# Kernel tuning notes

Hardware: AMD Instinct MI355X
Metric: run time of the kernel (lower is better)

Reference implementation:

```python
import jax, jax.numpy as jnp
import numpy as np

R_S, R_T = 16, 8
D_SEG, D_GLB = 64, 128
H_SEG, H_GLB = 2, 4
NL = 2
FF_SEG, FF_GLB = 128, 256
THRESH = 0.5
B, L = 16, 1024


def setup_inputs() -> dict:
    key = jax.random.key(0)
    ks = iter(jax.random.split(key, 40))

    def p(shape, s=0.02):
        return s * jax.random.normal(next(ks), shape, dtype=jnp.float32)

    inp = {}
    inp['pts'] = jax.random.normal(next(ks), (B, L, 3), dtype=jnp.float32)
    # Fourier spatio-temporal encoder params
    inp['fs'] = p((2, R_S), 1.0)                      # spatial frequencies
    inp['ft'] = p((R_T,), 1.0)                        # temporal frequencies
    inp['w_space'] = p((2 * R_S, D_SEG)); inp['b_space'] = p((D_SEG,))
    inp['w_time'] = p((2 * R_T, 32)); inp['b_time'] = p((32,))
    inp['w_fout'] = p((D_SEG + 32, D_SEG)); inp['b_fout'] = p((D_SEG,))
    # gating
    inp['w_gate'] = p((D_SEG,), 1.0); inp['b_gate'] = p(())
    # segment mini-transformer (2 post-norm encoder layers, relu FFN)
    inp['seg_attn_w'] = p((NL, 4, D_SEG, D_SEG)); inp['seg_attn_b'] = p((NL, 4, D_SEG))
    inp['seg_ln_g'] = jnp.ones((NL, 2, D_SEG), jnp.float32)
    inp['seg_ln_b'] = jnp.zeros((NL, 2, D_SEG), jnp.float32)
    inp['seg_ff1_w'] = p((NL, D_SEG, FF_SEG)); inp['seg_ff1_b'] = p((NL, FF_SEG))
    inp['seg_ff2_w'] = p((NL, FF_SEG, D_SEG)); inp['seg_ff2_b'] = p((NL, D_SEG))
    # global aggregator transformer
    inp['glb_attn_w'] = p((NL, 4, D_GLB, D_GLB)); inp['glb_attn_b'] = p((NL, 4, D_GLB))
    inp['glb_ln_g'] = jnp.ones((NL, 2, D_GLB), jnp.float32)
    inp['glb_ln_b'] = jnp.zeros((NL, 2, D_GLB), jnp.float32)
    inp['glb_ff1_w'] = p((NL, D_GLB, FF_GLB)); inp['glb_ff1_b'] = p((NL, FF_GLB))
    inp['glb_ff2_w'] = p((NL, FF_GLB, D_GLB)); inp['glb_ff2_b'] = p((NL, D_GLB))
    # projections
    inp['up_w'] = p((D_SEG, D_GLB)); inp['up_b'] = p((D_GLB,))
    inp['fin_w'] = p((D_GLB, D_GLB)); inp['fin_b'] = p((D_GLB,))
    return inp


def _ln(x, g, b, eps=1e-5):
    m = x.mean(-1, keepdims=True)
    v = ((x - m) ** 2).mean(-1, keepdims=True)
    return (x - m) * jax.lax.rsqrt(v + eps) * g + b


def _mha(x, mask, w, bb, nh):
    Bb, S, D = x.shape
    hd = D // nh
    wq, wk, wv, wo = w
    bq, bk, bv, bo = bb
    q = (x @ wq + bq).reshape(Bb, S, nh, hd)
    k = (x @ wk + bk).reshape(Bb, S, nh, hd)
    v = (x @ wv + bv).reshape(Bb, S, nh, hd)
    sc = jnp.einsum('bqhd,bkhd->bhqk', q, k) / jnp.sqrt(jnp.float32(hd))
    sc = jnp.where(mask[:, None, :, :], sc, jnp.float32(-1e9))
    a = jax.nn.softmax(sc, axis=-1)
    o = jnp.einsum('bhqk,bkhd->bqhd', a, v).reshape(Bb, S, D)
    return o @ wo + bo


def _encoder(x, mask, attn_w, attn_b, ln_g, ln_b, ff1_w, ff1_b, ff2_w, ff2_b, nh):
    # PyTorch-style post-norm TransformerEncoder (dropout=0, eval mode)
    for l in range(attn_w.shape[0]):
        x = _ln(x + _mha(x, mask, attn_w[l], attn_b[l], nh), ln_g[l, 0], ln_b[l, 0])
        h = jax.nn.relu(x @ ff1_w[l] + ff1_b[l]) @ ff2_w[l] + ff2_b[l]
        x = _ln(x + h, ln_g[l, 1], ln_b[l, 1])
    return x


def reference(pts, fs, ft, w_space, b_space, w_time, b_time, w_fout, b_fout, w_gate, b_gate, seg_attn_w, seg_attn_b, seg_ln_g, seg_ln_b, seg_ff1_w, seg_ff1_b, seg_ff2_w, seg_ff2_b, glb_attn_w, glb_attn_b, glb_ln_g, glb_ln_b, glb_ff1_w, glb_ff1_b, glb_ff2_w, glb_ff2_b, up_w, up_b, fin_w, fin_b):
    Bb, Ll, _ = pts.shape
    two_pi = jnp.float32(2.0 * np.pi)
    xy, t = pts[..., :2], pts[..., 2:3]
    # Fourier features (space + time), fused into d=64 point embedding z
    sp = xy @ fs * two_pi                                        # [B,L,r_s]
    sp_feat = jnp.concatenate([jnp.sin(sp), jnp.cos(sp)], -1) @ w_space + b_space
    tp = t * ft * two_pi                                         # [B,L,r_t]
    t_feat = jnp.concatenate([jnp.sin(tp), jnp.cos(tp)], -1) @ w_time + b_time
    z = jnp.concatenate([sp_feat, t_feat], -1) @ w_fout + b_fout  # [B,L,64]

    # dynamic segmentation gating: boundary where sigmoid gate > threshold
    gate = jax.nn.sigmoid(z @ w_gate + b_gate)                   # [B,L]
    boundary = (gate > THRESH).at[:, 0].set(True)
    seg_id = jnp.cumsum(boundary.astype(jnp.int32), axis=1) - 1  # [B,L] contiguous ids
    n_seg = seg_id[:, -1] + 1                                    # [B]

    # segment mini-transformer == full-length transformer with within-segment attention mask
    seg_mask = seg_id[:, :, None] == seg_id[:, None, :]          # [B,L,L]
    h = _encoder(z, seg_mask, seg_attn_w, seg_attn_b, seg_ln_g, seg_ln_b,
                 seg_ff1_w, seg_ff1_b, seg_ff2_w, seg_ff2_b, H_SEG)

    # per-segment mean pooling (padded to L segment slots)
    sums = jax.vmap(lambda hh, sid: jax.ops.segment_sum(hh, sid, num_segments=Ll))(h, seg_id)
    cnts = jax.vmap(lambda sid: jax.ops.segment_sum(jnp.ones((Ll,), jnp.float32), sid, num_segments=Ll))(seg_id)
    seg_emb = sums / jnp.maximum(cnts, 1.0)[..., None]           # [B,L,64]
    valid = jnp.arange(Ll)[None, :] < n_seg[:, None]             # [B,L]
    seg_emb = jnp.where(valid[..., None], seg_emb @ up_w + up_b, 0.0)  # [B,L,128]

    # global aggregator over valid segment embeddings (padding-masked)
    glb_mask = (valid[:, None, :] & valid[:, :, None]) | jnp.eye(Ll, dtype=bool)[None]
    g = _encoder(seg_emb, glb_mask, glb_attn_w, glb_attn_b, glb_ln_g, glb_ln_b,
                 glb_ff1_w, glb_ff1_b, glb_ff2_w, glb_ff2_b, H_GLB)
    agg = (g * valid[..., None]).sum(1) / n_seg[:, None].astype(jnp.float32)

    # single-segment trajectories skip the global aggregator
    global_emb = jnp.where((n_seg == 1)[:, None], seg_emb[:, 0, :], agg)
    return global_emb @ fin_w + fin_b                            # [B,128]
```

## Files before the change

kernel.cpp:

```cpp
#include <hip/hip_runtime.h>
#include <math.h>

#define B_ 16
#define L_ 1024
#define M_TOT (B_*L_)

typedef __attribute__((ext_vector_type(8))) short short8v;
typedef __attribute__((ext_vector_type(4))) float f32x4;

__device__ __forceinline__ float wave_reduce_sum(float v) {
#pragma unroll
  for (int o = 32; o >= 1; o >>= 1) v += __shfl_xor(v, o, 64);
  return v;
}

__device__ __forceinline__ unsigned short f2bf(float f) {
  union { float f; unsigned u; } v; v.f = f;
  unsigned r = v.u + 0x7FFFu + ((v.u >> 16) & 1u);
  return (unsigned short)(r >> 16);
}

__global__ __launch_bounds__(256) void pack_all_kernel(
    const float* __restrict__ s0, const float* __restrict__ s1,
    const float* __restrict__ s2, const float* __restrict__ s3,
    const float* __restrict__ s4, const float* __restrict__ s5,
    const float* __restrict__ s6, unsigned short* __restrict__ wpk)
{
  int idx = blockIdx.x*256 + (int)threadIdx.x;
  const float* src; unsigned short* dst; int K, N;
  if      (idx <  4096) { src=s0; dst=wpk;          K=64;  N=64;  }
  else if (idx <  6144) { src=s1; dst=wpk+32768;    K=64;  N=128; idx-=4096; }
  else if (idx <  8192) { src=s2; dst=wpk+49152;    K=128; N=64;  idx-=6144; }
  else if (idx < 24576) { src=s3; dst=wpk+65536;    K=128; N=128; idx-=8192; }
  else if (idx < 32768) { src=s4; dst=wpk+196608;   K=128; N=256; idx-=24576; }
  else if (idx < 40960) { src=s5; dst=wpk+262144;   K=256; N=128; idx-=32768; }
  else if (idx < 41984) { src=s6; dst=wpk+327680;   K=64;  N=128; idx-=40960; }
  else return;
  const int l = idx & 63;
  int f = idx >> 6;
  const int ntn = N >> 4;
  const int nt = f % ntn; f /= ntn;
  const int ktn = K >> 5;
  const int kt = f % ktn;
  const int m  = f / ktn;
  const float* s = src + (size_t)m*K*N + (size_t)(kt*32 + ((l>>4)<<3))*N + nt*16 + (l&15);
  unsigned pw[4];
#pragma unroll
  for (int jj = 0; jj < 4; ++jj)
    pw[jj] = (unsigned)f2bf(s[(size_t)(2*jj)*N]) | ((unsigned)f2bf(s[(size_t)(2*jj+1)*N]) << 16);
  uint4 u; u.x = pw[0]; u.y = pw[1]; u.z = pw[2]; u.w = pw[3];
  *reinterpret_cast<uint4*>(dst + (size_t)idx*8) = u;
}

template<int K, int PN, int NPARTS, bool RELU, bool GATED, bool WF32, bool WBF,
         int SPART = -1, bool SEMB0 = false>
__global__ __launch_bounds__(256) void mgemm_kernel(
    const unsigned short* __restrict__ Abf,
    const unsigned short* __restrict__ Wpk,
    const float* __restrict__ bias,
    float* __restrict__ C, unsigned short* __restrict__ Cbf,
    const int* __restrict__ nseg, float* __restrict__ semb0)
{
  constexpr int NOUT = NPARTS*PN;
  constexpr int KT = K/32;
  constexpr int NTP = PN/16;
  constexpr int CPP = PN/64;
  const int row0 = blockIdx.x * 64;
  if (GATED) { const int b = row0 >> 10; if ((row0 & (L_-1)) >= nseg[b]) return; }
  const int ct = blockIdx.y;
  const int part = ct / CPP;
  const int nt0  = (ct % CPP) * 4;
  const int wv = (int)threadIdx.x >> 6;
  const int ln = (int)threadIdx.x & 63;
  const int rbase = row0 + wv*16;
  const unsigned short* aptr = Abf + (size_t)(rbase + (ln & 15))*K + ((ln >> 4) << 3);
  const unsigned short* bptr = Wpk + ((size_t)part*KT*NTP + nt0)*512 + (size_t)ln*8;
  f32x4 acc0 = {0.f,0.f,0.f,0.f}, acc1 = {0.f,0.f,0.f,0.f};
  f32x4 acc2 = {0.f,0.f,0.f,0.f}, acc3 = {0.f,0.f,0.f,0.f};
#pragma unroll
  for (int kt = 0; kt < KT; ++kt) {
    short8v a = *reinterpret_cast<const short8v*>(aptr + kt*32);
    const unsigned short* bk = bptr + (size_t)kt*NTP*512;
    short8v b0 = *reinterpret_cast<const short8v*>(bk);
    short8v b1 = *reinterpret_cast<const short8v*>(bk + 512);
    short8v b2 = *reinterpret_cast<const short8v*>(bk + 1024);
    short8v b3 = *reinterpret_cast<const short8v*>(bk + 1536);
    acc0 = __builtin_amdgcn_mfma_f32_16x16x32_bf16(a, b0, acc0, 0, 0, 0);
    acc1 = __builtin_amdgcn_mfma_f32_16x16x32_bf16(a, b1, acc1, 0, 0, 0);
    acc2 = __builtin_amdgcn_mfma_f32_16x16x32_bf16(a, b2, acc2, 0, 0, 0);
    acc3 = __builtin_amdgcn_mfma_f32_16x16x32_bf16(a, b3, acc3, 0, 0, 0);
  }
  const int colb = part*PN + nt0*16 + (ln & 15);
  const int rowe = rbase + ((ln >> 4) << 2);
  f32x4 av[4] = {acc0, acc1, acc2, acc3};
#pragma unroll
  for (int i = 0; i < 4; ++i) {
    const int col = colb + i*16;
    const float bs = bias[col];
#pragma unroll
    for (int r = 0; r < 4; ++r) {
      float v = av[i][r] + bs;
      if (SPART >= 0) { if (part == SPART) v *= 0.25506972533f; }
      if (RELU) v = fmaxf(v, 0.f);
      const int row = rowe + r;
      if (WF32) C[(size_t)row*NOUT + col] = v;
      if (WBF)  Cbf[(size_t)row*NOUT + col] = f2bf(v);
      if (SEMB0) { if ((row & (L_-1)) == 0) semb0[(row >> 10)*NOUT + col] = v; }
    }
  }
}

__global__ __launch_bounds__(256) void mgemm_qkvfrag_kernel(
    const unsigned short* __restrict__ Abf,
    const unsigned short* __restrict__ Wpk,
    const float* __restrict__ bias,
    unsigned short* __restrict__ qbf,
    unsigned short* __restrict__ kfrag,
    unsigned short* __restrict__ vfrag,
    const int* __restrict__ nseg)
{
  constexpr int K = 128, PN = 128, KT = 4, NTP = 8;
  const int row0 = blockIdx.x * 64;
  const int bb = row0 >> 10;
  if ((row0 & (L_-1)) >= nseg[bb]) return;
  const int ct = blockIdx.y;
  const int part = ct >> 1;
  const int nt0 = (ct & 1) * 4;
  const int wv = (int)threadIdx.x >> 6;
  const int ln = (int)threadIdx.x & 63;
  const int qc = ln & 15;
  const int rbase = row0 + wv*16;
  const unsigned short* aptr = Abf + (size_t)(rbase + qc)*K + ((ln >> 4) << 3);
  const unsigned short* bptr = Wpk + ((size_t)part*KT*NTP + nt0)*512 + (size_t)ln*8;
  f32x4 acc[4];
#pragma unroll
  for (int i = 0; i < 4; ++i) acc[i] = f32x4{0.f,0.f,0.f,0.f};
#pragma unroll
  for (int kt = 0; kt < KT; ++kt) {
    short8v a = *reinterpret_cast<const short8v*>(aptr + kt*32);
    const unsigned short* bk = bptr + (size_t)kt*NTP*512;
#pragma unroll
    for (int i = 0; i < 4; ++i)
      acc[i] = __builtin_amdgcn_mfma_f32_16x16x32_bf16(
          a, *reinterpret_cast<const short8v*>(bk + i*512), acc[i], 0, 0, 0);
  }
  const int rowe = rbase + ((ln >> 4) << 2);
#pragma unroll
  for (int i = 0; i < 4; ++i) {
    const int cl = (nt0 + i)*16 + qc;
    const int h = cl >> 5, dh = cl & 31;
    const float bs = bias[part*PN + cl];
#pragma unroll
    for (int r = 0; r < 4; ++r) {
      float v = acc[i][r] + bs;
      const int row = rowe + r;
      const int key = row & (L_-1);
      if (part == 0) {
        v *= 0.25506972533f;
        qbf[(size_t)row*128 + cl] = f2bf(v);
      } else if (part == 1) {
        const size_t idx = (((size_t)((bb*4 + h)*32 + (key>>5))*2 + ((key>>4)&1))*64
                            + ((dh>>3)*16 + (key&15)))*8 + (dh&7);
        kfrag[idx] = f2bf(v);
      } else {
        const int kk = key & 31;
        const size_t idx = (((size_t)((bb*4 + h)*32 + (key>>5))*2 + (dh>>4))*64
                            + (((kk&15)>>2)*16 + (dh&15)))*8 + ((kk>>4)*4 + (kk&3));
        vfrag[idx] = f2bf(v);
      }
    }
  }
}

template<int K>
__global__ __launch_bounds__(256) void mgemm_ln64_kernel(
    const unsigned short* __restrict__ Abf,
    const unsigned short* __restrict__ Wpk,
    const float* __restrict__ bias,
    float* __restrict__ x,
    const float* __restrict__ gam, const float* __restrict__ bet,
    unsigned short* __restrict__ xbf)
{
  constexpr int KT = K/32;
  const int row0 = blockIdx.x * 64;
  const int wv = (int)threadIdx.x >> 6;
  const int ln = (int)threadIdx.x & 63;
  const int rbase = row0 + wv*16;
  const unsigned short* aptr = Abf + (size_t)(rbase + (ln & 15))*K + ((ln >> 4) << 3);
  const unsigned short* bptr = Wpk + (size_t)ln*8;
  f32x4 acc0 = {0.f,0.f,0.f,0.f}, acc1 = {0.f,0.f,0.f,0.f};
  f32x4 acc2 = {0.f,0.f,0.f,0.f}, acc3 = {0.f,0.f,0.f,0.f};
#pragma unroll
  for (int kt = 0; kt < KT; ++kt) {
    short8v a = *reinterpret_cast<const short8v*>(aptr + kt*32);
    const unsigned short* bk = bptr + (size_t)kt*4*512;
    short8v b0 = *reinterpret_cast<const short8v*>(bk);
    short8v b1 = *reinterpret_cast<const short8v*>(bk + 512);
    short8v b2 = *reinterpret_cast<const short8v*>(bk + 1024);
    short8v b3 = *reinterpret_cast<const short8v*>(bk + 1536);
    acc0 = __builtin_amdgcn_mfma_f32_16x16x32_bf16(a, b0, acc0, 0, 0, 0);
    acc1 = __builtin_amdgcn_mfma_f32_16x16x32_bf16(a, b1, acc1, 0, 0, 0);
    acc2 = __builtin_amdgcn_mfma_f32_16x16x32_bf16(a, b2, acc2, 0, 0, 0);
    acc3 = __builtin_amdgcn_mfma_f32_16x16x32_bf16(a, b3, acc3, 0, 0, 0);
  }
  const int colc = ln & 15;
  const int rowe = rbase + ((ln >> 4) << 2);
  f32x4 av[4] = {acc0, acc1, acc2, acc3};
  float v[4][4];
#pragma unroll
  for (int i = 0; i < 4; ++i) {
    const int col = i*16 + colc;
    const float bs = bias[col];
#pragma unroll
    for (int r = 0; r < 4; ++r)
      v[i][r] = av[i][r] + bs + x[(size_t)(rowe + r)*64 + col];
  }
  float rs[4];
#pragma unroll
  for (int r = 0; r < 4; ++r) rs[r] = v[0][r]+v[1][r]+v[2][r]+v[3][r];
#pragma unroll
  for (int m = 1; m <= 8; m <<= 1)
#pragma unroll
    for (int r = 0; r < 4; ++r) rs[r] += __shfl_xor(rs[r], m, 64);
  float mean[4], vs[4];
#pragma unroll
  for (int r = 0; r < 4; ++r) { mean[r] = rs[r]*(1.0f/64.0f); vs[r] = 0.f; }
#pragma unroll
  for (int i = 0; i < 4; ++i)
#pragma unroll
    for (int r = 0; r < 4; ++r) { const float d = v[i][r]-mean[r]; vs[r] = fmaf(d, d, vs[r]); }
#pragma unroll
  for (int m = 1; m <= 8; m <<= 1)
#pragma unroll
    for (int r = 0; r < 4; ++r) vs[r] += __shfl_xor(vs[r], m, 64);
  float rstd[4];
#pragma unroll
  for (int r = 0; r < 4; ++r) rstd[r] = rsqrtf(vs[r]*(1.0f/64.0f) + 1e-5f);
#pragma unroll
  for (int i = 0; i < 4; ++i) {
    const int col = i*16 + colc;
    const float g = gam[col], bb = bet[col];
#pragma unroll
    for (int r = 0; r < 4; ++r) {
      const float out = (v[i][r]-mean[r])*rstd[r]*g + bb;
      x[(size_t)(rowe + r)*64 + col] = out;
      xbf[(size_t)(rowe + r)*64 + col] = f2bf(out);
    }
  }
}

template<int K>
__global__ __launch_bounds__(256) void mgemm_ln128_kernel(
    const unsigned short* __restrict__ Abf,
    const unsigned short* __restrict__ Wpk,
    const float* __restrict__ bias,
    float* __restrict__ x,
    const float* __restrict__ gam, const float* __restrict__ bet,
    const int* __restrict__ nseg, unsigned short* __restrict__ xbf)
{
  constexpr int KT = K/32;
  const int row0 = blockIdx.x * 64;
  if ((row0 & (L_-1)) >= nseg[row0 >> 10]) return;
  const int wv = (int)threadIdx.x >> 6;
  const int ln = (int)threadIdx.x & 63;
  const int qc = ln & 15;
  const int rbase = row0 + wv*16;
  const unsigned short* aptr = Abf + (size_t)(rbase + qc)*K + ((ln >> 4) << 3);
  const unsigned short* bptr = Wpk + (size_t)ln*8;
  f32x4 acc[8];
#pragma unroll
  for (int i = 0; i < 8; ++i) acc[i] = f32x4{0.f,0.f,0.f,0.f};
#pragma unroll
  for (int kt = 0; kt < KT; ++kt) {
    short8v a = *reinterpret_cast<const short8v*>(aptr + kt*32);
    const unsigned short* bk = bptr + (size_t)kt*8*512;
#pragma unroll
    for (int i = 0; i < 8; ++i)
      acc[i] = __builtin_amdgcn_mfma_f32_16x16x32_bf16(
          a, *reinterpret_cast<const short8v*>(bk + i*512), acc[i], 0, 0, 0);
  }
  const int rowe = rbase + ((ln >> 4) << 2);
  float v[8][4];
#pragma unroll
  for (int i = 0; i < 8; ++i) {
    const int col = i*16 + qc;
    const float bs = bias[col];
#pragma unroll
    for (int r = 0; r < 4; ++r)
      v[i][r] = acc[i][r] + bs + x[(size_t)(rowe + r)*128 + col];
  }
  float rs[4];
#pragma unroll
  for (int r = 0; r < 4; ++r)
    rs[r] = ((v[0][r]+v[1][r])+(v[2][r]+v[3][r])) + ((v[4][r]+v[5][r])+(v[6][r]+v[7][r]));
#pragma unroll
  for (int m = 1; m <= 8; m <<= 1)
#pragma unroll
    for (int r = 0; r < 4; ++r) rs[r] += __shfl_xor(rs[r], m, 64);
  float mean[4], vs[4];
#pragma unroll
  for (int r = 0; r < 4; ++r) { mean[r] = rs[r]*(1.0f/128.0f); vs[r] = 0.f; }
#pragma unroll
  for (int i = 0; i < 8; ++i)
#pragma unroll
    for (int r = 0; r < 4; ++r) { const float d = v[i][r]-mean[r]; vs[r] = fmaf(d, d, vs[r]); }
#pragma unroll
  for (int m = 1; m <= 8; m <<= 1)
#pragma unroll
    for (int r = 0; r < 4; ++r) vs[r] += __shfl_xor(vs[r], m, 64);
  float rstd[4];
#pragma unroll
  for (int r = 0; r < 4; ++r) rstd[r] = rsqrtf(vs[r]*(1.0f/128.0f) + 1e-5f);
#pragma unroll
  for (int i = 0; i < 8; ++i) {
    const int col = i*16 + qc;
    const float g = gam[col], bb = bet[col];
#pragma unroll
    for (int r = 0; r < 4; ++r) {
      const float out = (v[i][r]-mean[r])*rstd[r]*g + bb;
      x[(size_t)(rowe + r)*128 + col] = out;
      xbf[(size_t)(rowe + r)*128 + col] = f2bf(out);
    }
  }
}

__global__ __launch_bounds__(256) void featurize_kernel(
    const float* __restrict__ pts, const float* __restrict__ fs, const float* __restrict__ ft,
    const float* __restrict__ w_space, const float* __restrict__ b_space,
    const float* __restrict__ w_time, const float* __restrict__ b_time,
    const float* __restrict__ w_fout, const float* __restrict__ b_fout,
    const float* __restrict__ w_gate, const float* __restrict__ b_gate,
    float* __restrict__ z, unsigned short* __restrict__ zbf, int* __restrict__ boundary)
{
  const int sub = threadIdx.x >> 6;
  const int d   = threadIdx.x & 63;
  const int p   = blockIdx.x * 4 + sub;
  const float TWO_PI = 6.283185307179586f;
  __shared__ float feat[4][32];
  __shared__ float tfeat[4][16];
  __shared__ float g96[4][96];
  const float x = pts[p*3+0], y = pts[p*3+1], t = pts[p*3+2];
  if (d < 16) {
    float sp = (x*fs[d] + y*fs[16+d]) * TWO_PI;
    feat[sub][d]    = sinf(sp);
    feat[sub][16+d] = cosf(sp);
  } else if (d < 24) {
    int r = d - 16;
    float tp = t * ft[r] * TWO_PI;
    tfeat[sub][r]   = sinf(tp);
    tfeat[sub][8+r] = cosf(tp);
  }
  __syncthreads();
  float sf = b_space[d];
#pragma unroll
  for (int k2 = 0; k2 < 32; ++k2) sf = fmaf(feat[sub][k2], w_space[k2*64+d], sf);
  g96[sub][d] = sf;
  if (d < 32) {
    float tf = b_time[d];
#pragma unroll
    for (int k2 = 0; k2 < 16; ++k2) tf = fmaf(tfeat[sub][k2], w_time[k2*32+d], tf);
    g96[sub][64+d] = tf;
  }
  __syncthreads();
  float zv = b_fout[d];
#pragma unroll
  for (int k2 = 0; k2 < 96; ++k2) zv = fmaf(g96[sub][k2], w_fout[k2*64+d], zv);
  z[(size_t)p*64+d] = zv;
  zbf[(size_t)p*64+d] = f2bf(zv);
  float gv = wave_reduce_sum(zv * w_gate[d]);
  if (d == 0) {
    float logit = gv + b_gate[0];
    float gate = 1.0f / (1.0f + expf(-logit));
    int bnd = (gate > 0.5f) ? 1 : 0;
    if ((p & (L_-1)) == 0) bnd = 1;
    boundary[p] = bnd;
  }
}

__global__ __launch_bounds__(1024) void scan_kernel(const int* __restrict__ boundary,
    int* __restrict__ seg_id, int* __restrict__ seg_start, int* __restrict__ n_seg)
{
  __shared__ int sc[1024];
  const int b = blockIdx.x, l = threadIdx.x;
  const int v = boundary[b*L_ + l];
  sc[l] = v;
  __syncthreads();
  for (int off = 1; off < 1024; off <<= 1) {
    int add = (l >= off) ? sc[l - off] : 0;
    __syncthreads();
    sc[l] += add;
    __syncthreads();
  }
  const int sid = sc[l] - 1;
  seg_id[b*L_ + l] = sid;
  if (v) seg_start[b*(L_+1) + sid] = l;
  if (l == L_-1) {
    n_seg[b] = sid + 1;
    seg_start[b*(L_+1) + sid + 1] = L_;
  }
}

__global__ __launch_bounds__(256) void seg_attn_kernel(
    const float* __restrict__ qkv,
    const int* __restrict__ seg_id, const int* __restrict__ seg_start,
    unsigned short* __restrict__ aobf)
{
  const int gid = blockIdx.x * 256 + (int)threadIdx.x;
  const int sub = gid & 7;
  const int item = gid >> 3;
  const int h  = item & 1;
  const int pt = (item >> 1) & (L_-1);
  const int b  = item >> 11;
  const float scale = 0.17677669529663687f;
  float4 q4 = *reinterpret_cast<const float4*>(qkv + (size_t)(b*L_+pt)*192 + h*32 + sub*4);
  q4.x*=scale; q4.y*=scale; q4.z*=scale; q4.w*=scale;
  const int s  = seg_id[b*L_ + pt];
  const int j0 = seg_start[b*(L_+1) + s];
  const int j1 = seg_start[b*(L_+1) + s + 1];
  float lsum = 0.f;
  float4 acc = {0.f,0.f,0.f,0.f};
  for (int j = j0; j < j1; ++j) {
    const float* base = qkv + (size_t)(b*L_ + j)*192 + h*32 + sub*4;
    float4 k4 = *reinterpret_cast<const float4*>(base + 64);
    float4 v4 = *reinterpret_cast<const float4*>(base + 128);
    float dot = q4.x*k4.x;
    dot = fmaf(q4.y, k4.y, dot);
    dot = fmaf(q4.z, k4.z, dot);
    dot = fmaf(q4.w, k4.w, dot);
    dot += __shfl_xor(dot, 1, 64);
    dot += __shfl_xor(dot, 2, 64);
    dot += __shfl_xor(dot, 4, 64);
    const float p = __expf(fminf(dot, 30.f));
    lsum += p;
    acc.x = fmaf(p, v4.x, acc.x);
    acc.y = fmaf(p, v4.y, acc.y);
    acc.z = fmaf(p, v4.z, acc.z);
    acc.w = fmaf(p, v4.w, acc.w);
  }
  const float inv = 1.0f / lsum;
  unsigned* op = reinterpret_cast<unsigned*>(aobf + (size_t)(b*L_+pt)*64 + h*32 + sub*4);
  op[0] = (unsigned)f2bf(acc.x*inv) | ((unsigned)f2bf(acc.y*inv) << 16);
  op[1] = (unsigned)f2bf(acc.z*inv) | ((unsigned)f2bf(acc.w*inv) << 16);
}

__global__ __launch_bounds__(256) void glb_attn_mfma_kernel(
    const unsigned short* __restrict__ qbf,
    const unsigned short* __restrict__ kfrag,
    const unsigned short* __restrict__ vfrag,
    const int* __restrict__ n_seg,
    unsigned short* __restrict__ aobf)
{
  const int g64 = blockIdx.x & 63;
  const int qt  = blockIdx.x >> 6;
  const int h  = g64 & 3;
  const int b  = g64 >> 2;
  const int ns = n_seg[b];
  if (qt*64 >= ns) return;
  const int wv = (int)threadIdx.x >> 6;
  const int ln = (int)threadIdx.x & 63;
  const int g  = ln >> 4;
  const int qc = ln & 15;
  __shared__ float lsumS[4][16];

  const int q0 = qt*64 + wv*16;
  const short8v qf = *reinterpret_cast<const short8v*>(
      qbf + (size_t)(b*L_ + q0 + qc)*128 + h*32 + g*8);

  f32x4 O0 = {0.f,0.f,0.f,0.f}, O1 = {0.f,0.f,0.f,0.f};
  const f32x4 zz = {0.f,0.f,0.f,0.f};
  float lsum = 0.f;
  const unsigned short* kfb = kfrag + (size_t)((b*4 + h)*32)*1024 + (size_t)ln*8;
  const unsigned short* vfb = vfrag + (size_t)((b*4 + h)*32)*1024 + (size_t)ln*8;

  const int nfull = ns >> 5;
#pragma unroll 2
  for (int c = 0; c < nfull; ++c) {
    short8v kf0 = *reinterpret_cast<const short8v*>(kfb);
    short8v kf1 = *reinterpret_cast<const short8v*>(kfb + 512);
    short8v v0  = *reinterpret_cast<const short8v*>(vfb);
    short8v v1  = *reinterpret_cast<const short8v*>(vfb + 512);
    f32x4 s0 = __builtin_amdgcn_mfma_f32_16x16x32_bf16(kf0, qf, zz, 0, 0, 0);
    f32x4 s1 = __builtin_amdgcn_mfma_f32_16x16x32_bf16(kf1, qf, zz, 0, 0, 0);
    float p[8];
#pragma unroll
    for (int r = 0; r < 4; ++r) {
      const float e0 = exp2f(fminf(s0[r], 43.f));
      const float e1 = exp2f(fminf(s1[r], 43.f));
      p[r] = e0; p[4+r] = e1;
      lsum += e0 + e1;
    }
    short8v pf;
#pragma unroll
    for (int i = 0; i < 8; ++i) pf[i] = (short)f2bf(p[i]);
    O0 = __builtin_amdgcn_mfma_f32_16x16x32_bf16(pf, v0, O0, 0, 0, 0);
    O1 = __builtin_amdgcn_mfma_f32_16x16x32_bf16(pf, v1, O1, 0, 0, 0);
    kfb += 1024; vfb += 1024;
  }
  if (ns & 31) {
    short8v kf0 = *reinterpret_cast<const short8v*>(kfb);
    short8v kf1 = *reinterpret_cast<const short8v*>(kfb + 512);
    short8v v0  = *reinterpret_cast<const short8v*>(vfb);
    short8v v1  = *reinterpret_cast<const short8v*>(vfb + 512);
    f32x4 s0 = __builtin_amdgcn_mfma_f32_16x16x32_bf16(kf0, qf, zz, 0, 0, 0);
    f32x4 s1 = __builtin_amdgcn_mfma_f32_16x16x32_bf16(kf1, qf, zz, 0, 0, 0);
    const int k0 = nfull*32;
    float p[8];
#pragma unroll
    for (int r = 0; r < 4; ++r) {
      const int key0 = k0 + g*4 + r;
      const float e0 = (key0 < ns)      ? exp2f(fminf(s0[r], 43.f)) : 0.f;
      const float e1 = (key0 + 16 < ns) ? exp2f(fminf(s1[r], 43.f)) : 0.f;
      p[r] = e0; p[4+r] = e1;
      lsum += e0 + e1;
    }
    short8v pf;
#pragma unroll
    for (int i = 0; i < 8; ++i) pf[i] = (short)f2bf(p[i]);
    O0 = __builtin_amdgcn_mfma_f32_16x16x32_bf16(pf, v0, O0, 0, 0, 0);
    O1 = __builtin_amdgcn_mfma_f32_16x16x32_bf16(pf, v1, O1, 0, 0, 0);
  }
  lsum += __shfl_xor(lsum, 16, 64);
  lsum += __shfl_xor(lsum, 32, 64);
  if (ln < 16) lsumS[wv][ln] = lsum;
  __syncthreads();
  unsigned short* outp = aobf + (size_t)(b*L_ + q0 + g*4)*128 + h*32 + qc;
#pragma unroll
  for (int r = 0; r < 4; ++r) {
    const float inv = 1.0f / lsumS[wv][g*4 + r];
    outp[(size_t)r*128]      = f2bf(O0[r]*inv);
    outp[(size_t)r*128 + 16] = f2bf(O1[r]*inv);
  }
}

__global__ __launch_bounds__(256) void pool_kernel(
    const float* __restrict__ h, const int* __restrict__ seg_start,
    const int* __restrict__ n_seg, unsigned short* __restrict__ meanbf)
{
  const int gs = blockIdx.x*4 + ((int)threadIdx.x >> 6);
  const int b = gs >> 10, s = gs & (L_-1);
  const int d = (int)threadIdx.x & 63;
  if (s >= n_seg[b]) return;
  const int j0 = seg_start[b*(L_+1)+s], j1 = seg_start[b*(L_+1)+s+1];
  float acc = 0.f;
  for (int j = j0; j < j1; ++j) acc += h[(size_t)(b*L_+j)*64 + d];
  meanbf[(size_t)gs*64 + d] = f2bf(acc / (float)(j1 - j0));
}

__global__ __launch_bounds__(128) void pool_final_kernel(
    const float* __restrict__ g, const int* __restrict__ n_seg,
    float* __restrict__ partial)
{
  const int b = blockIdx.x >> 4, c = blockIdx.x & 15;
  const int d = (int)threadIdx.x;
  const int ns = n_seg[b];
  const int i0 = c*64, i1 = min(ns, i0 + 64);
  float acc = 0.f;
  for (int i = i0; i < i1; ++i) acc += g[(size_t)(b*L_+i)*128 + d];
  partial[(size_t)blockIdx.x*128 + d] = acc;
}

__global__ __launch_bounds__(128) void final_kernel(
    const float* __restrict__ partial, const float* __restrict__ semb0,
    const int* __restrict__ n_seg, const float* __restrict__ fin_w,
    const float* __restrict__ fin_b, float* __restrict__ out)
{
  const int b = blockIdx.x, d = threadIdx.x;
  const int ns = n_seg[b];
  __shared__ float pl[128];
  float pooled;
  if (ns == 1) pooled = semb0[b*128 + d];
  else {
    float acc = 0.f;
#pragma unroll
    for (int c = 0; c < 16; ++c) acc += partial[(size_t)(b*16 + c)*128 + d];
    pooled = acc / (float)ns;
  }
  pl[d] = pooled;
  __syncthreads();
  float o = fin_b[d];
#pragma unroll 8
  for (int k2 = 0; k2 < 128; ++k2) o = fmaf(pl[k2], fin_w[k2*128+d], o);
  out[b*128+d] = o;
}

extern "C" void kernel_launch(void* const* d_in, const int* in_sizes, int n_in,
                              void* d_out, int out_size, void* d_ws, size_t ws_size,
                              hipStream_t stream) {
  const float* pts     = (const float*)d_in[0];
  const float* fs      = (const float*)d_in[1];
  const float* ft      = (const float*)d_in[2];
  const float* w_space = (const float*)d_in[3];
  const float* b_space = (const float*)d_in[4];
  const float* w_time  = (const float*)d_in[5];
  const float* b_time  = (const float*)d_in[6];
  const float* w_fout  = (const float*)d_in[7];
  const float* b_fout  = (const float*)d_in[8];
  const float* w_gate  = (const float*)d_in[9];
  const float* b_gate  = (const float*)d_in[10];
  const float* seg_attn_w = (const float*)d_in[11];
  const float* seg_attn_b = (const float*)d_in[12];
  const float* seg_ln_g   = (const float*)d_in[13];
  const float* seg_ln_b   = (const float*)d_in[14];
  const float* seg_ff1_w  = (const float*)d_in[15];
  const float* seg_ff1_b  = (const float*)d_in[16];
  const float* seg_ff2_w  = (const float*)d_in[17];
  const float* seg_ff2_b  = (const float*)d_in[18];
  const float* glb_attn_w = (const float*)d_in[19];
  const float* glb_attn_b = (const float*)d_in[20];
  const float* glb_ln_g   = (const float*)d_in[21];
  const float* glb_ln_b   = (const float*)d_in[22];
  const float* glb_ff1_w  = (const float*)d_in[23];
  const float* glb_ff1_b  = (const float*)d_in[24];
  const float* glb_ff2_w  = (const float*)d_in[25];
  const float* glb_ff2_b  = (const float*)d_in[26];
  const float* up_w    = (const float*)d_in[27];
  const float* up_b    = (const float*)d_in[28];
  const float* fin_w   = (const float*)d_in[29];
  const float* fin_b   = (const float*)d_in[30];

  char* ws = (char*)d_ws;
  float* zx   = (float*)(ws);
  unsigned short* xg_bf = (unsigned short*)(ws);
  float* qkv  = (float*)(ws + ((size_t)4  << 20));
  float* xg   = (float*)(ws + ((size_t)38 << 20));
  unsigned short* zx_bf = (unsigned short*)(ws + ((size_t)38 << 20));
  int* boundary  = (int*)(ws + ((size_t)46 << 20));
  int* seg_id    = boundary + M_TOT;
  int* seg_start = seg_id + M_TOT;
  int* n_seg     = seg_start + B_*(L_+1);
  float* semb0     = (float*)(ws + ((size_t)47 << 20));
  float* partial   = (float*)(ws + ((size_t)47 << 20) + 65536);
  unsigned short* tmp_bf = (unsigned short*)(ws + ((size_t)50 << 20));
  unsigned short* vfrag  = (unsigned short*)(ws + ((size_t)58 << 20));
  unsigned short* kfrag  = (unsigned short*)(ws + ((size_t)62 << 20));
  unsigned short* qbf    = (unsigned short*)(ws + ((size_t)66 << 20));
  unsigned short* abf    = (unsigned short*)(ws + ((size_t)84 << 20));
  unsigned short* wpk    = (unsigned short*)(ws + ((size_t)88 << 20));

  unsigned short* wpk_segA  = wpk;
  unsigned short* wpk_segF1 = wpk + 32768;
  unsigned short* wpk_segF2 = wpk + 49152;
  unsigned short* wpk_glbA  = wpk + 65536;
  unsigned short* wpk_glbF1 = wpk + 196608;
  unsigned short* wpk_glbF2 = wpk + 262144;
  unsigned short* wpk_up    = wpk + 327680;

  pack_all_kernel<<<164, 256, 0, stream>>>(seg_attn_w, seg_ff1_w, seg_ff2_w,
                                           glb_attn_w, glb_ff1_w, glb_ff2_w, up_w, wpk);

  featurize_kernel<<<M_TOT/4, 256, 0, stream>>>(pts, fs, ft, w_space, b_space, w_time, b_time,
                                                w_fout, b_fout, w_gate, b_gate, zx, zx_bf, boundary);
  scan_kernel<<<B_, 1024, 0, stream>>>(boundary, seg_id, seg_start, n_seg);

  for (int l = 0; l < 2; ++l) {
    const float* ab = seg_attn_b + (size_t)l*4*64;
    mgemm_kernel<64,64,3,false,false,true,false><<<dim3(256,3),256,0,stream>>>(
        zx_bf, wpk_segA + (size_t)l*4*4096, ab, qkv, nullptr, nullptr, nullptr);
    seg_attn_kernel<<<(M_TOT*2*8)/256, 256, 0, stream>>>(qkv, seg_id, seg_start, abf);
    mgemm_ln64_kernel<64><<<256,256,0,stream>>>(
        abf, wpk_segA + (size_t)(l*4+3)*4096, ab + 192,
        zx, seg_ln_g + l*128, seg_ln_b + l*128, zx_bf);
    mgemm_kernel<64,128,1,true,false,false,true><<<dim3(256,2),256,0,stream>>>(
        zx_bf, wpk_segF1 + (size_t)l*8192, seg_ff1_b + l*128, nullptr, tmp_bf, nullptr, nullptr);
    mgemm_ln64_kernel<128><<<256,256,0,stream>>>(
        tmp_bf, wpk_segF2 + (size_t)l*8192, seg_ff2_b + l*64,
        zx, seg_ln_g + l*128 + 64, seg_ln_b + l*128 + 64, zx_bf);
  }

  pool_kernel<<<M_TOT/4, 256, 0, stream>>>(zx, seg_start, n_seg, abf);
  mgemm_kernel<64,128,1,false,true,true,true,-1,true><<<dim3(256,2),256,0,stream>>>(
      abf, wpk_up, up_b, xg, xg_bf, n_seg, semb0);

  for (int l = 0; l < 2; ++l) {
    const float* ab = glb_attn_b + (size_t)l*4*128;
    mgemm_qkvfrag_kernel<<<dim3(256,6),256,0,stream>>>(
        xg_bf, wpk_glbA + (size_t)l*4*16384, ab, qbf, kfrag, vfrag, n_seg);
    glb_attn_mfma_kernel<<<B_*4*16, 256, 0, stream>>>(qbf, kfrag, vfrag, n_seg, abf);
    mgemm_ln128_kernel<128><<<256,256,0,stream>>>(
        abf, wpk_glbA + (size_t)(l*4+3)*16384, ab + 384,
        xg, glb_ln_g + l*256, glb_ln_b + l*256, n_seg, xg_bf);
    mgemm_kernel<128,256,1,true,true,false,true><<<dim3(256,4),256,0,stream>>>(
        xg_bf, wpk_glbF1 + (size_t)l*32768, glb_ff1_b + l*256, nullptr, tmp_bf, n_seg, nullptr);
    mgemm_ln128_kernel<256><<<256,256,0,stream>>>(
        tmp_bf, wpk_glbF2 + (size_t)l*32768, glb_ff2_b + l*128,
        xg, glb_ln_g + l*256 + 128, glb_ln_b + l*256 + 128, n_seg, xg_bf);
  }

  pool_final_kernel<<<B_*16, 128, 0, stream>>>(xg, n_seg, partial);
  final_kernel<<<B_, 128, 0, stream>>>(partial, semb0, n_seg, fin_w, fin_b, (float*)d_out);
}
```

Before: 237.2 us.

## Fuse FFN up/down GEMMs with LayerNorm and merge final pooling kernels

Adds fused segment and global FFN kernels. Each computes the first GEMM with ReLU into LDS as bf16, then runs the second GEMM plus residual and LayerNorm in the same block, so the intermediate activation never goes to global memory and one launch per layer is removed. The final mean-pooling and output projection are merged into one 1024-thread kernel that reduces partial sums in shared memory. The cost is more LDS and registers per block, which may lower occupancy, and the final kernel runs only 16 blocks.

```diff
diff --git a/kernel.cpp b/kernel.cpp
--- a/kernel.cpp
+++ b/kernel.cpp
@@ -288,6 +288,204 @@
 #pragma unroll
     for (int r = 0; r < 4; ++r)
       v[i][r] = acc[i][r] + bs + x[(size_t)(rowe + r)*128 + col];
+  }
+  float rs[4];
+#pragma unroll
+  for (int r = 0; r < 4; ++r)
+    rs[r] = ((v[0][r]+v[1][r])+(v[2][r]+v[3][r])) + ((v[4][r]+v[5][r])+(v[6][r]+v[7][r]));
+#pragma unroll
+  for (int m = 1; m <= 8; m <<= 1)
+#pragma unroll
+    for (int r = 0; r < 4; ++r) rs[r] += __shfl_xor(rs[r], m, 64);
+  float mean[4], vs[4];
+#pragma unroll
+  for (int r = 0; r < 4; ++r) { mean[r] = rs[r]*(1.0f/128.0f); vs[r] = 0.f; }
+#pragma unroll
+  for (int i = 0; i < 8; ++i)
+#pragma unroll
+    for (int r = 0; r < 4; ++r) { const float d = v[i][r]-mean[r]; vs[r] = fmaf(d, d, vs[r]); }
+#pragma unroll
+  for (int m = 1; m <= 8; m <<= 1)
+#pragma unroll
+    for (int r = 0; r < 4; ++r) vs[r] += __shfl_xor(vs[r], m, 64);
+  float rstd[4];
+#pragma unroll
+  for (int r = 0; r < 4; ++r) rstd[r] = rsqrtf(vs[r]*(1.0f/128.0f) + 1e-5f);
+#pragma unroll
+  for (int i = 0; i < 8; ++i) {
+    const int col = i*16 + qc;
+    const float g = gam[col], bb = bet[col];
+#pragma unroll
+    for (int r = 0; r < 4; ++r) {
+      const float out = (v[i][r]-mean[r])*rstd[r]*g + bb;
+      x[(size_t)(rowe + r)*128 + col] = out;
+      xbf[(size_t)(rowe + r)*128 + col] = f2bf(out);
+    }
+  }
+}
+
+__global__ __launch_bounds__(256) void seg_ff_kernel(
+    const unsigned short* __restrict__ Abf,
+    const unsigned short* __restrict__ W1,
+    const float* __restrict__ b1,
+    const unsigned short* __restrict__ W2,
+    const float* __restrict__ b2,
+    float* __restrict__ x, const float* __restrict__ gam, const float* __restrict__ bet,
+    unsigned short* __restrict__ xbf)
+{
+  __shared__ unsigned short HS[64][136];
+  const int row0 = blockIdx.x * 64;
+  const int wv = (int)threadIdx.x >> 6;
+  const int ln = (int)threadIdx.x & 63;
+  const int rbase = row0 + wv*16;
+  {
+    const unsigned short* aptr = Abf + (size_t)(rbase + (ln & 15))*64 + ((ln >> 4) << 3);
+    const unsigned short* bptr = W1 + (size_t)ln*8;
+    f32x4 acc[8];
+#pragma unroll
+    for (int i = 0; i < 8; ++i) acc[i] = f32x4{0.f,0.f,0.f,0.f};
+#pragma unroll
+    for (int kt = 0; kt < 2; ++kt) {
+      short8v a = *reinterpret_cast<const short8v*>(aptr + kt*32);
+      const unsigned short* bk = bptr + (size_t)kt*8*512;
+#pragma unroll
+      for (int i = 0; i < 8; ++i)
+        acc[i] = __builtin_amdgcn_mfma_f32_16x16x32_bf16(
+            a, *reinterpret_cast<const short8v*>(bk + i*512), acc[i], 0, 0, 0);
+    }
+    const int rl = wv*16 + ((ln >> 4) << 2);
+#pragma unroll
+    for (int i = 0; i < 8; ++i) {
+      const int col = i*16 + (ln & 15);
+      const float bs = b1[col];
+#pragma unroll
+      for (int r = 0; r < 4; ++r)
+        HS[rl + r][col] = f2bf(fmaxf(acc[i][r] + bs, 0.f));
+    }
+  }
+  __syncthreads();
+  const int rowl = wv*16 + (ln & 15);
+  f32x4 acc2[4];
+#pragma unroll
+  for (int i = 0; i < 4; ++i) acc2[i] = f32x4{0.f,0.f,0.f,0.f};
+#pragma unroll
+  for (int kt = 0; kt < 4; ++kt) {
+    short8v a = *reinterpret_cast<const short8v*>(&HS[rowl][kt*32 + ((ln >> 4) << 3)]);
+    const unsigned short* bk = W2 + (size_t)ln*8 + (size_t)kt*4*512;
+#pragma unroll
+    for (int i = 0; i < 4; ++i)
+      acc2[i] = __builtin_amdgcn_mfma_f32_16x16x32_bf16(
+          a, *reinterpret_cast<const short8v*>(bk + i*512), acc2[i], 0, 0, 0);
+  }
+  const int colc = ln & 15;
+  const int rowe = rbase + ((ln >> 4) << 2);
+  float v[4][4];
+#pragma unroll
+  for (int i = 0; i < 4; ++i) {
+    const int col = i*16 + colc;
+    const float bs = b2[col];
+#pragma unroll
+    for (int r = 0; r < 4; ++r)
+      v[i][r] = acc2[i][r] + bs + x[(size_t)(rowe + r)*64 + col];
+  }
+  float rs[4];
+#pragma unroll
+  for (int r = 0; r < 4; ++r) rs[r] = v[0][r]+v[1][r]+v[2][r]+v[3][r];
+#pragma unroll
+  for (int m = 1; m <= 8; m <<= 1)
+#pragma unroll
+    for (int r = 0; r < 4; ++r) rs[r] += __shfl_xor(rs[r], m, 64);
+  float mean[4], vs[4];
+#pragma unroll
+  for (int r = 0; r < 4; ++r) { mean[r] = rs[r]*(1.0f/64.0f); vs[r] = 0.f; }
+#pragma unroll
+  for (int i = 0; i < 4; ++i)
+#pragma unroll
+    for (int r = 0; r < 4; ++r) { const float d = v[i][r]-mean[r]; vs[r] = fmaf(d, d, vs[r]); }
+#pragma unroll
+  for (int m = 1; m <= 8; m <<= 1)
+#pragma unroll
+    for (int r = 0; r < 4; ++r) vs[r] += __shfl_xor(vs[r], m, 64);
+  float rstd[4];
+#pragma unroll
+  for (int r = 0; r < 4; ++r) rstd[r] = rsqrtf(vs[r]*(1.0f/64.0f) + 1e-5f);
+#pragma unroll
+  for (int i = 0; i < 4; ++i) {
+    const int col = i*16 + colc;
+    const float g = gam[col], bb = bet[col];
+#pragma unroll
+    for (int r = 0; r < 4; ++r) {
+      const float out = (v[i][r]-mean[r])*rstd[r]*g + bb;
+      x[(size_t)(rowe + r)*64 + col] = out;
+      xbf[(size_t)(rowe + r)*64 + col] = f2bf(out);
+    }
+  }
+}
+
+__global__ __launch_bounds__(256) void glb_ff_kernel(
+    const unsigned short* __restrict__ Abf,
+    const unsigned short* __restrict__ W1,
+    const float* __restrict__ b1,
+    const unsigned short* __restrict__ W2,
+    const float* __restrict__ b2,
+    float* __restrict__ x, const float* __restrict__ gam, const float* __restrict__ bet,
+    const int* __restrict__ nseg, unsigned short* __restrict__ xbf)
+{
+  __shared__ unsigned short HS[64][264];
+  const int row0 = blockIdx.x * 64;
+  if ((row0 & (L_-1)) >= nseg[row0 >> 10]) return;
+  const int wv = (int)threadIdx.x >> 6;
+  const int ln = (int)threadIdx.x & 63;
+  const int qc = ln & 15;
+  const int rbase = row0 + wv*16;
+  {
+    const unsigned short* aptr = Abf + (size_t)(rbase + qc)*128 + ((ln >> 4) << 3);
+    const unsigned short* bptr = W1 + (size_t)ln*8;
+    f32x4 acc[16];
+#pragma unroll
+    for (int i = 0; i < 16; ++i) acc[i] = f32x4{0.f,0.f,0.f,0.f};
+#pragma unroll
+    for (int kt = 0; kt < 4; ++kt) {
+      short8v a = *reinterpret_cast<const short8v*>(aptr + kt*32);
+      const unsigned short* bk = bptr + (size_t)kt*16*512;
+#pragma unroll
+      for (int i = 0; i < 16; ++i)
+        acc[i] = __builtin_amdgcn_mfma_f32_16x16x32_bf16(
+            a, *reinterpret_cast<const short8v*>(bk + i*512), acc[i], 0, 0, 0);
+    }
+    const int rl = wv*16 + ((ln >> 4) << 2);
+#pragma unroll
+    for (int i = 0; i < 16; ++i) {
+      const int col = i*16 + qc;
+      const float bs = b1[col];
+#pragma unroll
+      for (int r = 0; r < 4; ++r)
+        HS[rl + r][col] = f2bf(fmaxf(acc[i][r] + bs, 0.f));
+    }
+  }
+  __syncthreads();
+  const int rowl = wv*16 + qc;
+  f32x4 acc2[8];
+#pragma unroll
+  for (int i = 0; i < 8; ++i) acc2[i] = f32x4{0.f,0.f,0.f,0.f};
+#pragma unroll
+  for (int kt = 0; kt < 8; ++kt) {
+    short8v a = *reinterpret_cast<const short8v*>(&HS[rowl][kt*32 + ((ln >> 4) << 3)]);
+    const unsigned short* bk = W2 + (size_t)ln*8 + (size_t)kt*8*512;
+#pragma unroll
+    for (int i = 0; i < 8; ++i)
+      acc2[i] = __builtin_amdgcn_mfma_f32_16x16x32_bf16(
+          a, *reinterpret_cast<const short8v*>(bk + i*512), acc2[i], 0, 0, 0);
+  }
+  const int rowe = rbase + ((ln >> 4) << 2);
+  float v[8][4];
+#pragma unroll
+  for (int i = 0; i < 8; ++i) {
+    const int col = i*16 + qc;
+    const float bs = b2[col];
+#pragma unroll
+    for (int r = 0; r < 4; ++r)
+      v[i][r] = acc2[i][r] + bs + x[(size_t)(rowe + r)*128 + col];
   }
   float rs[4];
 #pragma unroll
@@ -546,41 +744,33 @@
   meanbf[(size_t)gs*64 + d] = f2bf(acc / (float)(j1 - j0));
 }
 
-__global__ __launch_bounds__(128) void pool_final_kernel(
-    const float* __restrict__ g, const int* __restrict__ n_seg,
-    float* __restrict__ partial)
-{
-  const int b = blockIdx.x >> 4, c = blockIdx.x & 15;
-  const int d = (int)threadIdx.x;
-  const int ns = n_seg[b];
-  const int i0 = c*64, i1 = min(ns, i0 + 64);
-  float acc = 0.f;
-  for (int i = i0; i < i1; ++i) acc += g[(size_t)(b*L_+i)*128 + d];
-  partial[(size_t)blockIdx.x*128 + d] = acc;
-}
-
-__global__ __launch_bounds__(128) void final_kernel(
-    const float* __restrict__ partial, const float* __restrict__ semb0,
+__global__ __launch_bounds__(1024) void final_kernel(
+    const float* __restrict__ g, const float* __restrict__ semb0,
     const int* __restrict__ n_seg, const float* __restrict__ fin_w,
     const float* __restrict__ fin_b, float* __restrict__ out)
 {
-  const int b = blockIdx.x, d = threadIdx.x;
+  const int b = blockIdx.x;
   const int ns = n_seg[b];
+  const int d = (int)threadIdx.x & 127;
+  const int c = (int)threadIdx.x >> 7;
+  __shared__ float part[8][128];
   __shared__ float pl[128];
-  float pooled;
-  if (ns == 1) pooled = semb0[b*128 + d];
-  else {
-    float acc = 0.f;
-#pragma unroll
-    for (int c = 0; c < 16; ++c) acc += partial[(size_t)(b*16 + c)*128 + d];
-    pooled = acc / (float)ns;
-  }
-  pl[d] = pooled;
+  float acc = 0.f;
+  for (int i = c; i < ns; i += 8) acc += g[(size_t)(b*L_+i)*128 + d];
+  part[c][d] = acc;
   __syncthreads();
-  float o = fin_b[d];
+  if (c == 0) {
+    float s = part[0][d]+part[1][d]+part[2][d]+part[3][d]
+            + part[4][d]+part[5][d]+part[6][d]+part[7][d];
+    pl[d] = (ns == 1) ? semb0[b*128 + d] : s / (float)ns;
+  }
+  __syncthreads();
+  if (c == 0) {
+    float o = fin_b[d];
 #pragma unroll 8
-  for (int k2 = 0; k2 < 128; ++k2) o = fmaf(pl[k2], fin_w[k2*128+d], o);
-  out[b*128+d] = o;
+    for (int k2 = 0; k2 < 128; ++k2) o = fmaf(pl[k2], fin_w[k2*128+d], o);
+    out[b*128+d] = o;
+  }
 }
 
 extern "C" void kernel_launch(void* const* d_in, const int* in_sizes, int n_in,
@@ -629,8 +819,6 @@
   int* seg_start = seg_id + M_TOT;
   int* n_seg     = seg_start + B_*(L_+1);
   float* semb0     = (float*)(ws + ((size_t)47 << 20));
-  float* partial   = (float*)(ws + ((size_t)47 << 20) + 65536);
-  unsigned short* tmp_bf = (unsigned short*)(ws + ((size_t)50 << 20));
   unsigned short* vfrag  = (unsigned short*)(ws + ((size_t)58 << 20));
   unsigned short* kfrag  = (unsigned short*)(ws + ((size_t)62 << 20));
   unsigned short* qbf    = (unsigned short*)(ws + ((size_t)66 << 20));
@@ -660,10 +848,9 @@
     mgemm_ln64_kernel<64><<<256,256,0,stream>>>(
         abf, wpk_segA + (size_t)(l*4+3)*4096, ab + 192,
         zx, seg_ln_g + l*128, seg_ln_b + l*128, zx_bf);
-    mgemm_kernel<64,128,1,true,false,false,true><<<dim3(256,2),256,0,stream>>>(
-        zx_bf, wpk_segF1 + (size_t)l*8192, seg_ff1_b + l*128, nullptr, tmp_bf, nullptr, nullptr);
-    mgemm_ln64_kernel<128><<<256,256,0,stream>>>(
-        tmp_bf, wpk_segF2 + (size_t)l*8192, seg_ff2_b + l*64,
+    seg_ff_kernel<<<256,256,0,stream>>>(
+        zx_bf, wpk_segF1 + (size_t)l*8192, seg_ff1_b + l*128,
+        wpk_segF2 + (size_t)l*8192, seg_ff2_b + l*64,
         zx, seg_ln_g + l*128 + 64, seg_ln_b + l*128 + 64, zx_bf);
   }
 
@@ -679,13 +866,11 @@
     mgemm_ln128_kernel<128><<<256,256,0,stream>>>(
         abf, wpk_glbA + (size_t)(l*4+3)*16384, ab + 384,
         xg, glb_ln_g + l*256, glb_ln_b + l*256, n_seg, xg_bf);
-    mgemm_kernel<128,256,1,true,true,false,true><<<dim3(256,4),256,0,stream>>>(
-        xg_bf, wpk_glbF1 + (size_t)l*32768, glb_ff1_b + l*256, nullptr, tmp_bf, n_seg, nullptr);
-    mgemm_ln128_kernel<256><<<256,256,0,stream>>>(
-        tmp_bf, wpk_glbF2 + (size_t)l*32768, glb_ff2_b + l*128,
+    glb_ff_kernel<<<256,256,0,stream>>>(
+        xg_bf, wpk_glbF1 + (size_t)l*32768, glb_ff1_b + l*256,
+        wpk_glbF2 + (size_t)l*32768, glb_ff2_b + l*128,
         xg, glb_ln_g + l*256 + 128, glb_ln_b + l*256 + 128, n_seg, xg_bf);
   }
 
-  pool_final_kernel<<<B_*16, 128, 0, stream>>>(xg, n_seg, partial);
-  final_kernel<<<B_, 128, 0, stream>>>(partial, semb0, n_seg, fin_w, fin_b, (float*)d_out);
-}
+  final_kernel<<<B_, 1024, 0, stream>>>(xg, semb0, n_seg, fin_w, fin_b, (float*)d_out);
+}
```

New measurement: 247.1 us. 4.2% more time.
